# Optimization experiments

Hardware: AMD Instinct MI355X
Metric: run time of the kernel (lower is better)

The kernel has to match this reference:

```python
import jax, jax.numpy as jnp
import numpy as np

B, S, H, K, E, C = 4, 1024, 1024, 8, 512, 10000

def setup_inputs() -> dict:
    key = jax.random.key(0)
    ks = jax.random.split(key, 5)
    context = jax.random.normal(ks[0], (B, S, H), dtype=jnp.float32)
    prior_w = jax.random.normal(ks[1], (K, H), dtype=jnp.float32) * 0.02
    prior_b = jnp.zeros((K,), dtype=jnp.float32)
    latent_w = jax.random.normal(ks[2], (K * E, H), dtype=jnp.float32) * 0.02
    latent_b = jnp.zeros((K * E,), dtype=jnp.float32)
    dec_w = jax.random.normal(ks[3], (C, E), dtype=jnp.float32) * 0.02
    dec_b = jnp.zeros((C,), dtype=jnp.float32)
    return {"context": context, "prior_w": prior_w, "prior_b": prior_b,
            "latent_w": latent_w, "latent_b": latent_b,
            "dec_w": dec_w, "dec_b": dec_b}

def reference(context, prior_w, prior_b, latent_w, latent_b, dec_w, dec_b):
    # priors: softmax over components  [B,S,K]
    priors = jax.nn.softmax(jnp.einsum('bsh,kh->bsk', context, prior_w) + prior_b, axis=-1)
    # latent: [B,S,K,E] after tanh (dropout is identity at inference, dropoutl=0)
    latent = jnp.tanh((jnp.einsum('bsh,eh->bse', context, latent_w) + latent_b)
                      .reshape(B, S, K, E))
    # decoder logits + per-component softmax over classes  [B,S,K,C]
    probs = jax.nn.softmax(jnp.einsum('bske,ce->bskc', latent, dec_w) + dec_b, axis=-1)
    # mixture-weighted sum over components  [B,S,C]
    return jnp.einsum('bsk,bskc->bsc', priors, probs)
```

## Files before the change

### kernel.cpp

```cpp
#include <hip/hip_runtime.h>
#include <hip/hip_bf16.h>


#define BM 128
#define BN 128
#define BK 64

typedef __attribute__((ext_vector_type(8))) short bf16x8;
typedef __attribute__((ext_vector_type(4))) float f32x4;
typedef __attribute__((ext_vector_type(8))) _Float16 f16x8;

typedef const __attribute__((address_space(1))) unsigned int* gas_u32p;
typedef __attribute__((address_space(3))) unsigned int* las_u32p;

__device__ __forceinline__ unsigned short f2bf(float x) {
  union { float f; unsigned int u; } un; un.f = x;
  unsigned int r = un.u + 0x7FFFu + ((un.u >> 16) & 1u);
  return (unsigned short)(r >> 16);
}

__global__ void k_cvt_bf16(const float4* __restrict__ src, ushort4* __restrict__ dst, int n4) {
  int i = blockIdx.x * blockDim.x + threadIdx.x;
  if (i < n4) {
    float4 v = src[i];
    ushort4 o;
    o.x = f2bf(v.x); o.y = f2bf(v.y); o.z = f2bf(v.z); o.w = f2bf(v.w);
    dst[i] = o;
  }
}

__global__ void k_priors(const float* __restrict__ ctx, const float* __restrict__ pw,
                         const float* __restrict__ pb, float* __restrict__ priors) {
  int t = blockIdx.x;
  int lane = threadIdx.x;
  __shared__ float logit[8];
  const float* c = ctx + (size_t)t * 1024;
  for (int k = 0; k < 8; ++k) {
    const float* w = pw + k * 1024;
    float s = 0.f;
    for (int h = lane; h < 1024; h += 64) s += c[h] * w[h];
    #pragma unroll
    for (int m = 1; m <= 32; m <<= 1) s += __shfl_xor(s, m);
    if (lane == 0) logit[k] = s + pb[k];
  }
  __syncthreads();
  if (lane == 0) {
    float mx = logit[0];
    for (int k = 1; k < 8; ++k) mx = fmaxf(mx, logit[k]);
    float z = 0.f, e[8];
    for (int k = 0; k < 8; ++k) { e[k] = __expf(logit[k] - mx); z += e[k]; }
    float inv = 1.f / z;
    for (int k = 0; k < 8; ++k) priors[(size_t)t * 8 + k] = e[k] * inv;
  }
}

__device__ __forceinline__ void gemm_mainloop(
    const unsigned short* __restrict__ A, const unsigned short* __restrict__ B,
    int lda, int ldb, int m0, int n0, int ktiles,
    unsigned short* ldsA, unsigned short* ldsB, f32x4 acc[4][4]) {
  const int tid = threadIdx.x;
  const int lane = tid & 63;
  const int wave = tid >> 6;
  const int wm = wave & 1, wn = wave >> 1;
  const int lrow = lane & 15, lq = lane >> 4;

  for (int kt = 0; kt < ktiles; ++kt) {
    int k0 = kt * BK;
    __syncthreads();
    #pragma unroll
    for (int p = 0; p < 4; ++p) {
      int chunk = p * 256 + tid;
      int row = chunk >> 3, kc = chunk & 7;
      int kcs = kc ^ (row & 7);
      __builtin_amdgcn_global_load_lds(
          (gas_u32p)(A + (size_t)(m0 + row) * lda + k0 + kcs * 8),
          (las_u32p)(ldsA + chunk * 8), 16, 0, 0);
      __builtin_amdgcn_global_load_lds(
          (gas_u32p)(B + (size_t)(n0 + row) * ldb + k0 + kcs * 8),
          (las_u32p)(ldsB + chunk * 8), 16, 0, 0);
    }
    __syncthreads();
    #pragma unroll
    for (int s = 0; s < 2; ++s) {
      int cbyteoff = (((s * 4 + lq) ^ (lrow & 7)) * 8);
      bf16x8 af[4], bfr[4];
      #pragma unroll
      for (int f = 0; f < 4; ++f)
        af[f] = *(const bf16x8*)(ldsA + (wm * 64 + f * 16 + lrow) * BK + cbyteoff);
      #pragma unroll
      for (int f = 0; f < 4; ++f)
        bfr[f] = *(const bf16x8*)(ldsB + (wn * 64 + f * 16 + lrow) * BK + cbyteoff);
      #pragma unroll
      for (int fi = 0; fi < 4; ++fi)
        #pragma unroll
        for (int fj = 0; fj < 4; ++fj)
          acc[fi][fj] = __builtin_amdgcn_mfma_f32_16x16x32_bf16(af[fi], bfr[fj], acc[fi][fj], 0, 0, 0);
    }
  }
}

__global__ __launch_bounds__(256, 4)
void k_latent(const unsigned short* __restrict__ ctxb, const unsigned short* __restrict__ lwb,
              const float* __restrict__ lb, unsigned short* __restrict__ latent) {
  __shared__ unsigned short lds[(BM + BN) * BK];
  f32x4 zero = {0.f, 0.f, 0.f, 0.f};
  f32x4 acc[4][4];
  #pragma unroll
  for (int i = 0; i < 4; ++i)
    #pragma unroll
    for (int j = 0; j < 4; ++j) acc[i][j] = zero;
  int l = blockIdx.x;
  int xcd = l & 7, idx = l >> 3;
  int ctl = idx & 3, by = idx >> 2;
  int m0 = by * BM, n0 = (xcd * 4 + ctl) * BN;
  gemm_mainloop(ctxb, lwb, 1024, 1024, m0, n0, 1024 / BK, lds, lds + BM * BK, acc);

  const int lane = threadIdx.x & 63, wave = threadIdx.x >> 6;
  const int wm = wave & 1, wn = wave >> 1, lrow = lane & 15, lq = lane >> 4;
  #pragma unroll
  for (int fi = 0; fi < 4; ++fi)
    #pragma unroll
    for (int fj = 0; fj < 4; ++fj) {
      int gcol = n0 + wn * 64 + fj * 16 + lrow;
      float bias = lb[gcol];
      #pragma unroll
      for (int r = 0; r < 4; ++r) {
        int grow = m0 + wm * 64 + fi * 16 + lq * 4 + r;
        float v = tanhf(acc[fi][fj][r] + bias);
        latent[(size_t)grow * 4096 + gcol] = f2bf(v);
      }
    }
}

template<int STORE>
__global__ __launch_bounds__(256, 4)
void k_dec_pass1(const unsigned short* __restrict__ latb, const unsigned short* __restrict__ dwb,
                 const float* __restrict__ db, float* __restrict__ Z,
                 _Float16* __restrict__ P, int m_base) {
  __shared__ unsigned short lds[(BM + BN) * BK];
  int l = blockIdx.x;
  int xcd = l & 7, idx = l >> 3;
  int ctl = idx % 10, by = idx / 10;
  int n0 = (xcd * 10 + ctl) * BN, m0 = m_base + by * BM;
  if (n0 >= 10000) return;

  f32x4 zero = {0.f, 0.f, 0.f, 0.f};
  f32x4 acc[4][4];
  #pragma unroll
  for (int i = 0; i < 4; ++i)
    #pragma unroll
    for (int j = 0; j < 4; ++j) acc[i][j] = zero;
  gemm_mainloop(latb, dwb, 512, 512, m0, n0, 512 / BK, lds, lds + BM * BK, acc);

  const int lane = threadIdx.x & 63, wave = threadIdx.x >> 6;
  const int wm = wave & 1, wn = wave >> 1, lrow = lane & 15, lq = lane >> 4;

  if (STORE) __syncthreads();
  _Float16* ldsP = (_Float16*)lds;

  float rowsum[4][4];
  #pragma unroll
  for (int fi = 0; fi < 4; ++fi)
    #pragma unroll
    for (int r = 0; r < 4; ++r) rowsum[fi][r] = 0.f;
  #pragma unroll
  for (int fj = 0; fj < 4; ++fj) {
    int gcol = n0 + wn * 64 + fj * 16 + lrow;
    bool valid = gcol < 10000;
    float bias = valid ? db[gcol] : 0.f;
    #pragma unroll
    for (int fi = 0; fi < 4; ++fi)
      #pragma unroll
      for (int r = 0; r < 4; ++r) {
        float e = __expf(acc[fi][fj][r] + bias);
        if (STORE) {
          _Float16 h = (_Float16)e;
          if (valid) rowsum[fi][r] += (float)h;
          int row_l = wm * 64 + fi * 16 + lq * 4 + r;
          int col_l = wn * 64 + fj * 16 + lrow;
          ldsP[row_l * 128 + (((col_l >> 3) ^ (row_l & 7)) << 3) + (col_l & 7)] = h;
        } else {
          if (valid) rowsum[fi][r] += e;
        }
      }
  }

  if (STORE) {
    __syncthreads();
    #pragma unroll
    for (int it = 0; it < 8; ++it) {
      int chunk = it * 256 + threadIdx.x;
      int row_l = chunk >> 4, c8 = chunk & 15;
      int slot = c8 ^ (row_l & 7);
      uint4 v = *(const uint4*)((const char*)lds + row_l * 256 + slot * 16);
      *(uint4*)(P + (size_t)(by * BM + row_l) * 10112 + n0 + c8 * 8) = v;
    }
  }

  #pragma unroll
  for (int fi = 0; fi < 4; ++fi)
    #pragma unroll
    for (int r = 0; r < 4; ++r) {
      float s = rowsum[fi][r];
      s += __shfl_xor(s, 1); s += __shfl_xor(s, 2);
      s += __shfl_xor(s, 4); s += __shfl_xor(s, 8);
      if (lrow == 0) atomicAdd(&Z[m0 + wm * 64 + fi * 16 + lq * 4 + r], s);
    }
}

__global__ __launch_bounds__(256)
void k_combine(const _Float16* __restrict__ P, const float* __restrict__ priors,
               const float* __restrict__ Z, float* __restrict__ out, int t_base) {
  int tl = blockIdx.x;
  int t  = t_base + tl;
  const _Float16* base = P + (size_t)tl * 8 * 10112;
  float w[8];
  #pragma unroll
  for (int k = 0; k < 8; ++k) w[k] = priors[t * 8 + k] / Z[t * 8 + k];
  int c8 = blockIdx.y * 256 + threadIdx.x;
  if (c8 < 1250) {
    int c = c8 * 8;
    float s[8] = {0.f, 0.f, 0.f, 0.f, 0.f, 0.f, 0.f, 0.f};
    #pragma unroll
    for (int k = 0; k < 8; ++k) {
      f16x8 v = *(const f16x8*)(base + (size_t)k * 10112 + c);
      #pragma unroll
      for (int j = 0; j < 8; ++j) s[j] += w[k] * (float)v[j];
    }
    float4 o0 = {s[0], s[1], s[2], s[3]};
    float4 o1 = {s[4], s[5], s[6], s[7]};
    *(float4*)(out + (size_t)t * 10000 + c) = o0;
    *(float4*)(out + (size_t)t * 10000 + c + 4) = o1;
  }
}

__global__ __launch_bounds__(256, 4)
void k_dec_pass2(const unsigned short* __restrict__ latb, const unsigned short* __restrict__ dwb,
                 const float* __restrict__ db, const float* __restrict__ priors,
                 const float* __restrict__ Z, float* __restrict__ out) {
  __shared__ unsigned short lds[(BM + BN) * BK];
  int l = blockIdx.x;
  int xcd = l & 7, idx = l >> 3;
  int ctl = idx % 10, by = idx / 10;
  int n0 = (xcd * 10 + ctl) * BN, m0 = by * BM;
  if (n0 >= 10000) return;

  f32x4 zero = {0.f, 0.f, 0.f, 0.f};
  f32x4 acc[4][4];
  #pragma unroll
  for (int i = 0; i < 4; ++i)
    #pragma unroll
    for (int j = 0; j < 4; ++j) acc[i][j] = zero;
  gemm_mainloop(latb, dwb, 512, 512, m0, n0, 512 / BK, lds, lds + BM * BK, acc);

  const int tid = threadIdx.x;
  const int lane = tid & 63, wave = tid >> 6;
  const int wm = wave & 1, wn = wave >> 1, lrow = lane & 15, lq = lane >> 4;

  __syncthreads();
  float* ldsO = (float*)lds;

  #pragma unroll
  for (int fi = 0; fi < 4; ++fi) {
    int rbase = m0 + wm * 64 + fi * 16 + lq * 4;
    float w[4];
    #pragma unroll
    for (int r = 0; r < 4; ++r) w[r] = priors[rbase + r] / Z[rbase + r];
    #pragma unroll
    for (int fj = 0; fj < 4; ++fj) {
      int gcol = n0 + wn * 64 + fj * 16 + lrow;
      float bias = (gcol < 10000) ? db[gcol] : 0.f;
      float part = 0.f;
      #pragma unroll
      for (int r = 0; r < 4; ++r) part += w[r] * __expf(acc[fi][fj][r] + bias);
      float tok = part + __shfl_xor(part, 16);
      if (!(lq & 1)) {
        int tl = wm * 8 + fi * 2 + (lq >> 1);
        int cl = wn * 64 + fj * 16 + lrow;
        ldsO[tl * 128 + cl] = tok;
      }
    }
  }
  __syncthreads();
  int tok0 = m0 >> 3;
  #pragma unroll
  for (int it = 0; it < 2; ++it) {
    int f = it * 256 + tid;
    int tl = f >> 5, c4 = f & 31;
    int col = n0 + c4 * 4;
    if (col < 10000)
      *(float4*)(out + (size_t)(tok0 + tl) * 10000 + col) = *(float4*)(ldsO + tl * 128 + c4 * 4);
  }
}

extern "C" void kernel_launch(void* const* d_in, const int* in_sizes, int n_in,
                              void* d_out, int out_size, void* d_ws, size_t ws_size,
                              hipStream_t stream) {
  const float* ctx = (const float*)d_in[0];
  const float* pw  = (const float*)d_in[1];
  const float* pb  = (const float*)d_in[2];
  const float* lw  = (const float*)d_in[3];
  const float* lb  = (const float*)d_in[4];
  const float* dw  = (const float*)d_in[5];
  const float* db  = (const float*)d_in[6];
  float* out = (float*)d_out;

  char* ws = (char*)d_ws;
  unsigned short* ctxb = (unsigned short*)ws;
  unsigned short* lwb  = (unsigned short*)(ws + 8388608);
  unsigned short* dwb  = (unsigned short*)(ws + 16777216);
  unsigned short* latb = (unsigned short*)(ws + 27131904);
  float* priors        = (float*)(ws + 60686336);
  float* Z             = (float*)(ws + 60817408);
  _Float16* Pex        = (_Float16*)(ws + 60948480);
  const size_t WS_BASE = 60948480ull;

  size_t avail = ws_size > WS_BASE ? ws_size - WS_BASE : 0;
  long long mrows_ll = (long long)(avail / (10112ull * 2ull)) & ~127ll;
  if (mrows_ll > 8192) mrows_ll = 8192;
  int mrows = (int)mrows_ll;
  int nch = mrows > 0 ? (32768 + mrows - 1) / mrows : 1000;
  const bool store_path = (nch <= 16);

  k_cvt_bf16<<<4096, 256, 0, stream>>>((const float4*)ctx, (ushort4*)ctxb, 1048576);
  k_cvt_bf16<<<4096, 256, 0, stream>>>((const float4*)lw,  (ushort4*)lwb,  1048576);
  k_cvt_bf16<<<5000, 256, 0, stream>>>((const float4*)dw,  (ushort4*)dwb,  1280000);
  hipMemsetAsync(dwb + (size_t)10000 * 512, 0, (size_t)112 * 512 * 2, stream);
  hipMemsetAsync(Z, 0, 32768 * 4, stream);

  k_priors<<<4096, 64, 0, stream>>>(ctx, pw, pb, priors);
  k_latent<<<1024, 256, 0, stream>>>(ctxb, lwb, lb, latb);
  if (store_path) {
    for (int ms = 0; ms < 32768; ms += mrows) {
      int rows = 32768 - ms < mrows ? 32768 - ms : mrows;
      k_dec_pass1<1><<<(rows / 128) * 80, 256, 0, stream>>>(latb, dwb, db, Z, Pex, ms);
      k_combine<<<dim3(rows / 8, 5), 256, 0, stream>>>(Pex, priors, Z, out, ms / 8);
    }
  } else {
    k_dec_pass1<0><<<20480, 256, 0, stream>>>(latb, dwb, db, Z, nullptr, 0);
    k_dec_pass2<<<20480, 256, 0, stream>>>(latb, dwb, db, priors, Z, out);
  }
}
```

Measured before the change: 1.003 ms.

## Fuse conversions, co-schedule priors with latent GEMM, and software-pipeline decoder chunks

Merges the three bf16 conversion launches into one kernel and interleaves the priors computation as odd blocks of the latent GEMM kernel. It also double-buffers the decoder exp buffer so that each launch runs pass1 for chunk i alongside the combine for chunk i-1. The goal is fewer launches and filling idle CUs that the memory-bound combine and priors phases leave behind. This needs twice the workspace and assumes pass1 for a chunk never races with the combine reading the other buffer.

```diff
diff --git a/kernel.cpp b/kernel.cpp
--- a/kernel.cpp
+++ b/kernel.cpp
@@ -19,37 +19,47 @@
   return (unsigned short)(r >> 16);
 }
 
-__global__ void k_cvt_bf16(const float4* __restrict__ src, ushort4* __restrict__ dst, int n4) {
-  int i = blockIdx.x * blockDim.x + threadIdx.x;
-  if (i < n4) {
-    float4 v = src[i];
-    ushort4 o;
-    o.x = f2bf(v.x); o.y = f2bf(v.y); o.z = f2bf(v.z); o.w = f2bf(v.w);
-    dst[i] = o;
-  }
-}
-
-__global__ void k_priors(const float* __restrict__ ctx, const float* __restrict__ pw,
-                         const float* __restrict__ pb, float* __restrict__ priors) {
-  int t = blockIdx.x;
-  int lane = threadIdx.x;
-  __shared__ float logit[8];
+__global__ void k_cvt_all(const float4* __restrict__ ctx, ushort4* __restrict__ ctxb,
+                          const float4* __restrict__ lw, ushort4* __restrict__ lwb,
+                          const float4* __restrict__ dw, ushort4* __restrict__ dwb) {
+  int i = blockIdx.x * 256 + threadIdx.x;
+  const float4* s; ushort4* d; int off;
+  if (i < 1048576) { s = ctx; d = ctxb; off = i; }
+  else if (i < 2097152) { s = lw; d = lwb; off = i - 1048576; }
+  else if (i < 3377152) { s = dw; d = dwb; off = i - 2097152; }
+  else return;
+  float4 v = s[off];
+  ushort4 o;
+  o.x = f2bf(v.x); o.y = f2bf(v.y); o.z = f2bf(v.z); o.w = f2bf(v.w);
+  d[off] = o;
+}
+
+__device__ __forceinline__ void priors_body(int pid, const float* __restrict__ ctx,
+                                            const float* __restrict__ pw,
+                                            const float* __restrict__ pb,
+                                            float* __restrict__ priors) {
+  int wave = threadIdx.x >> 6, lane = threadIdx.x & 63;
+  int t = pid * 4 + wave;
   const float* c = ctx + (size_t)t * 1024;
+  float lg[8];
+  #pragma unroll
   for (int k = 0; k < 8; ++k) {
     const float* w = pw + k * 1024;
     float s = 0.f;
     for (int h = lane; h < 1024; h += 64) s += c[h] * w[h];
     #pragma unroll
     for (int m = 1; m <= 32; m <<= 1) s += __shfl_xor(s, m);
-    if (lane == 0) logit[k] = s + pb[k];
-  }
-  __syncthreads();
+    lg[k] = s + pb[k];
+  }
   if (lane == 0) {
-    float mx = logit[0];
-    for (int k = 1; k < 8; ++k) mx = fmaxf(mx, logit[k]);
+    float mx = lg[0];
+    #pragma unroll
+    for (int k = 1; k < 8; ++k) mx = fmaxf(mx, lg[k]);
     float z = 0.f, e[8];
-    for (int k = 0; k < 8; ++k) { e[k] = __expf(logit[k] - mx); z += e[k]; }
+    #pragma unroll
+    for (int k = 0; k < 8; ++k) { e[k] = __expf(lg[k] - mx); z += e[k]; }
     float inv = 1.f / z;
+    #pragma unroll
     for (int k = 0; k < 8; ++k) priors[(size_t)t * 8 + k] = e[k] * inv;
   }
 }
@@ -99,18 +109,18 @@
   }
 }
 
-__global__ __launch_bounds__(256, 4)
-void k_latent(const unsigned short* __restrict__ ctxb, const unsigned short* __restrict__ lwb,
-              const float* __restrict__ lb, unsigned short* __restrict__ latent) {
-  __shared__ unsigned short lds[(BM + BN) * BK];
+__device__ __forceinline__ void latent_body(int id, const unsigned short* __restrict__ ctxb,
+                                            const unsigned short* __restrict__ lwb,
+                                            const float* __restrict__ lb,
+                                            unsigned short* __restrict__ latent,
+                                            unsigned short* lds) {
   f32x4 zero = {0.f, 0.f, 0.f, 0.f};
   f32x4 acc[4][4];
   #pragma unroll
   for (int i = 0; i < 4; ++i)
     #pragma unroll
     for (int j = 0; j < 4; ++j) acc[i][j] = zero;
-  int l = blockIdx.x;
-  int xcd = l & 7, idx = l >> 3;
+  int xcd = id & 7, idx = id >> 3;
   int ctl = idx & 3, by = idx >> 2;
   int m0 = by * BM, n0 = (xcd * 4 + ctl) * BN;
   gemm_mainloop(ctxb, lwb, 1024, 1024, m0, n0, 1024 / BK, lds, lds + BM * BK, acc);
@@ -131,6 +141,131 @@
       }
     }
 }
+
+__global__ __launch_bounds__(256, 4)
+void k_lat_pri(const unsigned short* __restrict__ ctxb, const unsigned short* __restrict__ lwb,
+               const float* __restrict__ lb, unsigned short* __restrict__ latent,
+               const float* __restrict__ ctx, const float* __restrict__ pw,
+               const float* __restrict__ pb, float* __restrict__ priors) {
+  __shared__ unsigned short lds[(BM + BN) * BK];
+  int l = blockIdx.x;
+  if (l & 1) { priors_body(l >> 1, ctx, pw, pb, priors); return; }
+  latent_body(l >> 1, ctxb, lwb, lb, latent, lds);
+}
+
+__device__ __forceinline__ void dec_pass1_body(int id, const unsigned short* __restrict__ latb,
+                                               const unsigned short* __restrict__ dwb,
+                                               const float* __restrict__ db,
+                                               float* __restrict__ Z,
+                                               _Float16* __restrict__ P, int m_base,
+                                               unsigned short* lds) {
+  int xcd = id & 7, idx = id >> 3;
+  int ctl = idx % 10, by = idx / 10;
+  int n0 = (xcd * 10 + ctl) * BN, m0 = m_base + by * BM;
+  if (n0 >= 10000) return;
+
+  f32x4 zero = {0.f, 0.f, 0.f, 0.f};
+  f32x4 acc[4][4];
+  #pragma unroll
+  for (int i = 0; i < 4; ++i)
+    #pragma unroll
+    for (int j = 0; j < 4; ++j) acc[i][j] = zero;
+  gemm_mainloop(latb, dwb, 512, 512, m0, n0, 512 / BK, lds, lds + BM * BK, acc);
+
+  const int lane = threadIdx.x & 63, wave = threadIdx.x >> 6;
+  const int wm = wave & 1, wn = wave >> 1, lrow = lane & 15, lq = lane >> 4;
+
+  __syncthreads();
+  _Float16* ldsP = (_Float16*)lds;
+
+  float rowsum[4][4];
+  #pragma unroll
+  for (int fi = 0; fi < 4; ++fi)
+    #pragma unroll
+    for (int r = 0; r < 4; ++r) rowsum[fi][r] = 0.f;
+  #pragma unroll
+  for (int fj = 0; fj < 4; ++fj) {
+    int gcol = n0 + wn * 64 + fj * 16 + lrow;
+    bool valid = gcol < 10000;
+    float bias = valid ? db[gcol] : 0.f;
+    #pragma unroll
+    for (int fi = 0; fi < 4; ++fi)
+      #pragma unroll
+      for (int r = 0; r < 4; ++r) {
+        float e = __expf(acc[fi][fj][r] + bias);
+        _Float16 h = (_Float16)e;
+        if (valid) rowsum[fi][r] += (float)h;
+        int row_l = wm * 64 + fi * 16 + lq * 4 + r;
+        int col_l = wn * 64 + fj * 16 + lrow;
+        ldsP[row_l * 128 + (((col_l >> 3) ^ (row_l & 7)) << 3) + (col_l & 7)] = h;
+      }
+  }
+
+  __syncthreads();
+  #pragma unroll
+  for (int it = 0; it < 8; ++it) {
+    int chunk = it * 256 + threadIdx.x;
+    int row_l = chunk >> 4, c8 = chunk & 15;
+    int slot = c8 ^ (row_l & 7);
+    uint4 v = *(const uint4*)((const char*)lds + row_l * 256 + slot * 16);
+    *(uint4*)(P + (size_t)(by * BM + row_l) * 10112 + n0 + c8 * 8) = v;
+  }
+
+  #pragma unroll
+  for (int fi = 0; fi < 4; ++fi)
+    #pragma unroll
+    for (int r = 0; r < 4; ++r) {
+      float s = rowsum[fi][r];
+      s += __shfl_xor(s, 1); s += __shfl_xor(s, 2);
+      s += __shfl_xor(s, 4); s += __shfl_xor(s, 8);
+      if (lrow == 0) atomicAdd(&Z[m0 + wm * 64 + fi * 16 + lq * 4 + r], s);
+    }
+}
+
+__device__ __forceinline__ void combine_body(int id, const _Float16* __restrict__ P,
+                                             const float* __restrict__ priors,
+                                             const float* __restrict__ Z,
+                                             float* __restrict__ out, int t_base) {
+  int tl = id / 5, yg = id % 5;
+  int t = t_base + tl;
+  const _Float16* base = P + (size_t)tl * 8 * 10112;
+  float w[8];
+  #pragma unroll
+  for (int k = 0; k < 8; ++k) w[k] = priors[t * 8 + k] / Z[t * 8 + k];
+  int c8 = yg * 256 + threadIdx.x;
+  if (c8 < 1250) {
+    int c = c8 * 8;
+    float s[8] = {0.f, 0.f, 0.f, 0.f, 0.f, 0.f, 0.f, 0.f};
+    #pragma unroll
+    for (int k = 0; k < 8; ++k) {
+      f16x8 v = *(const f16x8*)(base + (size_t)k * 10112 + c);
+      #pragma unroll
+      for (int j = 0; j < 8; ++j) s[j] += w[k] * (float)v[j];
+    }
+    float4 o0 = {s[0], s[1], s[2], s[3]};
+    float4 o1 = {s[4], s[5], s[6], s[7]};
+    *(float4*)(out + (size_t)t * 10000 + c) = o0;
+    *(float4*)(out + (size_t)t * 10000 + c + 4) = o1;
+  }
+}
+
+__global__ __launch_bounds__(256, 4)
+void k_dec_fat(const unsigned short* __restrict__ latb, const unsigned short* __restrict__ dwb,
+               const float* __restrict__ db, float* __restrict__ Z,
+               _Float16* __restrict__ Pw, int m_base,
+               const _Float16* __restrict__ Pr, const float* __restrict__ priors,
+               float* __restrict__ out, int t_base,
+               int n_p1, int n_cb) {
+  __shared__ unsigned short lds[(BM + BN) * BK];
+  int l = blockIdx.x;
+  bool cb; int id;
+  if (n_p1 == 0)      { cb = true;  id = l; }
+  else if (n_cb == 0) { cb = false; id = l; }
+  else                { cb = (l & 1); id = l >> 1; }
+  if (cb) { combine_body(id, Pr, priors, Z, out, t_base); return; }
+  dec_pass1_body(id, latb, dwb, db, Z, Pw, m_base, lds);
+}
+
 
 template<int STORE>
 __global__ __launch_bounds__(256, 4)
@@ -138,12 +273,15 @@
                  const float* __restrict__ db, float* __restrict__ Z,
                  _Float16* __restrict__ P, int m_base) {
   __shared__ unsigned short lds[(BM + BN) * BK];
+  if (STORE) {
+    dec_pass1_body(blockIdx.x, latb, dwb, db, Z, P, m_base, lds);
+    return;
+  }
   int l = blockIdx.x;
   int xcd = l & 7, idx = l >> 3;
   int ctl = idx % 10, by = idx / 10;
   int n0 = (xcd * 10 + ctl) * BN, m0 = m_base + by * BM;
   if (n0 >= 10000) return;
-
   f32x4 zero = {0.f, 0.f, 0.f, 0.f};
   f32x4 acc[4][4];
   #pragma unroll
@@ -151,13 +289,8 @@
     #pragma unroll
     for (int j = 0; j < 4; ++j) acc[i][j] = zero;
   gemm_mainloop(latb, dwb, 512, 512, m0, n0, 512 / BK, lds, lds + BM * BK, acc);
-
   const int lane = threadIdx.x & 63, wave = threadIdx.x >> 6;
   const int wm = wave & 1, wn = wave >> 1, lrow = lane & 15, lq = lane >> 4;
-
-  if (STORE) __syncthreads();
-  _Float16* ldsP = (_Float16*)lds;
-
   float rowsum[4][4];
   #pragma unroll
   for (int fi = 0; fi < 4; ++fi)
@@ -171,32 +304,9 @@
     #pragma unroll
     for (int fi = 0; fi < 4; ++fi)
       #pragma unroll
-      for (int r = 0; r < 4; ++r) {
-        float e = __expf(acc[fi][fj][r] + bias);
-        if (STORE) {
-          _Float16 h = (_Float16)e;
-          if (valid) rowsum[fi][r] += (float)h;
-          int row_l = wm * 64 + fi * 16 + lq * 4 + r;
-          int col_l = wn * 64 + fj * 16 + lrow;
-          ldsP[row_l * 128 + (((col_l >> 3) ^ (row_l & 7)) << 3) + (col_l & 7)] = h;
-        } else {
-          if (valid) rowsum[fi][r] += e;
-        }
-      }
-  }
-
-  if (STORE) {
-    __syncthreads();
-    #pragma unroll
-    for (int it = 0; it < 8; ++it) {
-      int chunk = it * 256 + threadIdx.x;
-      int row_l = chunk >> 4, c8 = chunk & 15;
-      int slot = c8 ^ (row_l & 7);
-      uint4 v = *(const uint4*)((const char*)lds + row_l * 256 + slot * 16);
-      *(uint4*)(P + (size_t)(by * BM + row_l) * 10112 + n0 + c8 * 8) = v;
-    }
-  }
-
+      for (int r = 0; r < 4; ++r)
+        if (valid) rowsum[fi][r] += __expf(acc[fi][fj][r] + bias);
+  }
   #pragma unroll
   for (int fi = 0; fi < 4; ++fi)
     #pragma unroll
@@ -211,27 +321,7 @@
 __global__ __launch_bounds__(256)
 void k_combine(const _Float16* __restrict__ P, const float* __restrict__ priors,
                const float* __restrict__ Z, float* __restrict__ out, int t_base) {
-  int tl = blockIdx.x;
-  int t  = t_base + tl;
-  const _Float16* base = P + (size_t)tl * 8 * 10112;
-  float w[8];
-  #pragma unroll
-  for (int k = 0; k < 8; ++k) w[k] = priors[t * 8 + k] / Z[t * 8 + k];
-  int c8 = blockIdx.y * 256 + threadIdx.x;
-  if (c8 < 1250) {
-    int c = c8 * 8;
-    float s[8] = {0.f, 0.f, 0.f, 0.f, 0.f, 0.f, 0.f, 0.f};
-    #pragma unroll
-    for (int k = 0; k < 8; ++k) {
-      f16x8 v = *(const f16x8*)(base + (size_t)k * 10112 + c);
-      #pragma unroll
-      for (int j = 0; j < 8; ++j) s[j] += w[k] * (float)v[j];
-    }
-    float4 o0 = {s[0], s[1], s[2], s[3]};
-    float4 o1 = {s[4], s[5], s[6], s[7]};
-    *(float4*)(out + (size_t)t * 10000 + c) = o0;
-    *(float4*)(out + (size_t)t * 10000 + c + 4) = o1;
-  }
+  combine_body(blockIdx.y + 5 * blockIdx.x, P, priors, Z, out, t_base);
 }
 
 __global__ __launch_bounds__(256, 4)
@@ -312,29 +402,37 @@
   unsigned short* latb = (unsigned short*)(ws + 27131904);
   float* priors        = (float*)(ws + 60686336);
   float* Z             = (float*)(ws + 60817408);
-  _Float16* Pex        = (_Float16*)(ws + 60948480);
   const size_t WS_BASE = 60948480ull;
+  const size_t CHUNK_BYTES = 8192ull * 10112ull * 2ull;
+  _Float16* pex[2] = { (_Float16*)(ws + WS_BASE),
+                       (_Float16*)(ws + WS_BASE + CHUNK_BYTES) };
 
   size_t avail = ws_size > WS_BASE ? ws_size - WS_BASE : 0;
-  long long mrows_ll = (long long)(avail / (10112ull * 2ull)) & ~127ll;
-  if (mrows_ll > 8192) mrows_ll = 8192;
-  int mrows = (int)mrows_ll;
-  int nch = mrows > 0 ? (32768 + mrows - 1) / mrows : 1000;
-  const bool store_path = (nch <= 16);
-
-  k_cvt_bf16<<<4096, 256, 0, stream>>>((const float4*)ctx, (ushort4*)ctxb, 1048576);
-  k_cvt_bf16<<<4096, 256, 0, stream>>>((const float4*)lw,  (ushort4*)lwb,  1048576);
-  k_cvt_bf16<<<5000, 256, 0, stream>>>((const float4*)dw,  (ushort4*)dwb,  1280000);
+  int mode = (avail >= 2 * CHUNK_BYTES) ? 2 : (avail >= CHUNK_BYTES ? 1 : 0);
+
+  k_cvt_all<<<13192, 256, 0, stream>>>((const float4*)ctx, (ushort4*)ctxb,
+                                       (const float4*)lw, (ushort4*)lwb,
+                                       (const float4*)dw, (ushort4*)dwb);
   hipMemsetAsync(dwb + (size_t)10000 * 512, 0, (size_t)112 * 512 * 2, stream);
   hipMemsetAsync(Z, 0, 32768 * 4, stream);
 
-  k_priors<<<4096, 64, 0, stream>>>(ctx, pw, pb, priors);
-  k_latent<<<1024, 256, 0, stream>>>(ctxb, lwb, lb, latb);
-  if (store_path) {
-    for (int ms = 0; ms < 32768; ms += mrows) {
-      int rows = 32768 - ms < mrows ? 32768 - ms : mrows;
-      k_dec_pass1<1><<<(rows / 128) * 80, 256, 0, stream>>>(latb, dwb, db, Z, Pex, ms);
-      k_combine<<<dim3(rows / 8, 5), 256, 0, stream>>>(Pex, priors, Z, out, ms / 8);
+  k_lat_pri<<<2048, 256, 0, stream>>>(ctxb, lwb, lb, latb, ctx, pw, pb, priors);
+
+  if (mode == 2) {
+    for (int ch = 0; ch < 5; ++ch) {
+      int n_p1 = (ch < 4) ? 5120 : 0;
+      int n_cb = (ch > 0) ? 5120 : 0;
+      k_dec_fat<<<n_p1 + n_cb, 256, 0, stream>>>(
+          latb, dwb, db, Z,
+          (ch < 4) ? pex[ch & 1] : nullptr, ch * 8192,
+          (ch > 0) ? pex[(ch - 1) & 1] : nullptr, priors,
+          out, (ch - 1) * 1024,
+          n_p1, n_cb);
+    }
+  } else if (mode == 1) {
+    for (int ms = 0; ms < 32768; ms += 8192) {
+      k_dec_pass1<1><<<5120, 256, 0, stream>>>(latb, dwb, db, Z, pex[0], ms);
+      k_combine<<<dim3(1024, 5), 256, 0, stream>>>(pex[0], priors, Z, out, ms / 8);
     }
   } else {
     k_dec_pass1<0><<<20480, 256, 0, stream>>>(latb, dwb, db, Z, nullptr, 0);
```

Measured after the change: 1.306 ms. 1.3x slower.
